# Kernel tuning notes

Hardware: AMD Instinct MI355X
Metric: run time of the kernel (lower is better)

Reference implementation:

```python
import jax, jax.numpy as jnp
import numpy as np

CODEBOOK_SIZE = 8192
CODEBOOK_DIM = 16
IN_DIM = 512


def setup_inputs() -> dict:
    key = jax.random.key(0)
    k1, k2, k3 = jax.random.split(key, 3)
    input_values = jax.random.normal(k1, (8, 4096, IN_DIM), dtype=jnp.float32)
    # xavier_uniform for Linear(IN_DIM -> CODEBOOK_DIM), weight shape (out, in) in torch
    limit = float(np.sqrt(6.0 / (IN_DIM + CODEBOOK_DIM)))
    proj_weight = jax.random.uniform(k2, (CODEBOOK_DIM, IN_DIM), dtype=jnp.float32, minval=-limit, maxval=limit)
    code_book = jax.random.normal(k3, (CODEBOOK_SIZE, CODEBOOK_DIM), dtype=jnp.float32)
    return {"input_values": input_values, "proj_weight": proj_weight, "code_book": code_book}


def reference(input_values, proj_weight, code_book):
    # targets: (B, L, d) = input @ W^T  (bias-free random projection)
    targets = jnp.einsum("bld,cd->blc", input_values, proj_weight)  # (B, L, 16)
    # Squared L2 distance via expansion ||t - c||^2 = ||t||^2 - 2 t.c + ||c||^2.
    # argmin is identical to argmin of the norm; avoids the (B,L,K,d) broadcast tensor.
    t_sq = jnp.sum(targets * targets, axis=-1, keepdims=True)        # (B, L, 1)
    c_sq = jnp.sum(code_book * code_book, axis=-1)                   # (K,)
    cross = jnp.einsum("blc,kc->blk", targets, code_book)            # (B, L, K)
    dist_sq = t_sq - 2.0 * cross + c_sq                              # (B, L, K)
    labels = jnp.argmin(dist_sq, axis=-1)                            # (B, L) int
    return labels
```

## Files before the change

kernel.cpp:

```cpp
#include <hip/hip_runtime.h>
#include <stdint.h>

#define IN_DIM 512
#define CB 8192
#define CD 16
#define NROWS 32768
#define DELTAQ 8e-3f
#define FMAXV 3.402823466e38f

typedef short bf16x8 __attribute__((ext_vector_type(8)));
typedef float f32x4 __attribute__((ext_vector_type(4)));

__device__ inline unsigned short f2bf(float x) {
    unsigned u = __float_as_uint(x);
    unsigned r = u + 0x7FFFu + ((u >> 16) & 1u);
    return (unsigned short)(r >> 16);
}
__device__ inline float bf2f(unsigned short h) { return __uint_as_float(((unsigned)h) << 16); }
__device__ inline unsigned umin32(unsigned a, unsigned b) { return a < b ? a : b; }
__device__ inline unsigned umax32(unsigned a, unsigned b) { return a > b ? a : b; }
__device__ inline unsigned long long shfl_xor_u64(unsigned long long x, int m) {
    double d = __shfl_xor(__longlong_as_double((long long)x), m, 64);
    return (unsigned long long)__double_as_longlong(d);
}
__device__ inline unsigned med3_u32(unsigned a, unsigned b, unsigned c) {
    unsigned d;
    asm("v_med3_u32 %0, %1, %2, %3" : "=v"(d) : "v"(a), "v"(b), "v"(c));
    return d;
}

__global__ __launch_bounds__(256) void prep_proj_kernel(const float* __restrict__ in,
                                                        const float* __restrict__ W,
                                                        float* __restrict__ partials,
                                                        const float* __restrict__ cb,
                                                        float* __restrict__ csq,
                                                        f32x4* __restrict__ csq4,
                                                        bf16x8* __restrict__ Bp,
                                                        int* __restrict__ counter) {
    __shared__ float4 LIN[2048];
    __shared__ float4 WL[16 * 33];
    int tid = threadIdx.x;

    if (blockIdx.x >= 2048) {
        int id = (blockIdx.x - 2048) * 256 + tid;
        if (id == 0) counter[0] = 0;
        if (id < CB) {
            const float4* p = (const float4*)(cb + (size_t)id * CD);
            float s = 0.f;
#pragma unroll
            for (int j = 0; j < 4; ++j) {
                float4 v = p[j];
                s += v.x * v.x + v.y * v.y + v.z * v.z + v.w * v.w;
            }
            csq[id] = s;
            float so = s + 256.0f;
            f32x4 v4 = {so, so, so, so};
            csq4[id] = v4;
        }
        int slot = id & 63;
        int nt = id >> 6;
        int q = slot >> 4;
        int n = nt * 16 + (slot & 15);
        int d0 = (q & 1) * 8;
        bool lo = (q < 2);
        const float* src = cb + (size_t)n * CD + d0;
        bf16x8 v;
#pragma unroll
        for (int j = 0; j < 8; ++j) {
            float x = src[j];
            unsigned short a = f2bf(x);
            unsigned short b = f2bf(x - bf2f(a));
            v[j] = (short)(lo ? a : b);
        }
        Bp[id] = v;
        return;
    }

    int lane = tid & 63;
    int dg = __builtin_amdgcn_readfirstlane(tid >> 6);
    int strip = blockIdx.x >> 2;
    int c = blockIdx.x & 3;
    int rowbase = strip * 64;
    const float4* inp4 = (const float4*)in;
    const float4* W4 = (const float4*)W;

#pragma unroll
    for (int u = 0; u < 2; ++u) {
        int f = tid + u * 256;
        int d = f >> 5, o = f & 31;
        WL[d * 33 + o] = W4[(size_t)d * 128 + c * 32 + o];
    }
#pragma unroll
    for (int u = 0; u < 8; ++u) {
        int f = tid + u * 256;
        int o = f & 31, r = f >> 5;
        LIN[o * 64 + (r ^ (o & 7))] = inp4[(size_t)(rowbase + r) * 128 + c * 32 + o];
    }
    __syncthreads();

    float acc[4];
#pragma unroll
    for (int i = 0; i < 4; ++i) acc[i] = 0.f;
#pragma unroll 4
    for (int j = 0; j < 32; ++j) {
        float4 v = LIN[j * 64 + (lane ^ (j & 7))];
#pragma unroll
        for (int i = 0; i < 4; ++i) {
            float4 w = WL[(4 * dg + i) * 33 + j];
            acc[i] += v.x * w.x + v.y * w.y + v.z * w.z + v.w * w.w;
        }
    }
    float* o = partials + (size_t)c * NROWS * CD + (size_t)(rowbase + lane) * CD + 4 * dg;
#pragma unroll
    for (int i = 0; i < 4; ++i) o[i] = acc[i];
}

__global__ __launch_bounds__(512, 4) void scan_kernel(
        const float* __restrict__ partials, const f32x4* __restrict__ csq4,
        const bf16x8* __restrict__ Bp, int* __restrict__ out,
        int* __restrict__ queue, int* __restrict__ counter) {
    __shared__ float tbuf[64][17];
    __shared__ unsigned long long m_k[64][8];
    __shared__ unsigned m_s2[64][8];

    int tid = threadIdx.x;
    int lane = tid & 63;
    int e = __builtin_amdgcn_readfirstlane(tid >> 6);
    int rowbase = blockIdx.x * 64;

#pragma unroll
    for (int u = 0; u < 2; ++u) {
        int f = tid + u * 512;
        int rr = f >> 4, d = f & 15;
        size_t idx = (size_t)(rowbase + rr) * CD + d;
        const size_t P = (size_t)NROWS * CD;
        float p0 = partials[idx];
        float p1 = partials[P + idx];
        float p2 = partials[2 * P + idx];
        float p3 = partials[3 * P + idx];
        tbuf[rr][d] = -2.f * (((p0 + p1) + p2) + p3);
    }
    __syncthreads();

    int q = lane >> 4;
    int col = lane & 15;
    int d0 = (q & 1) * 8;
    bool lo = (q < 2);

    bf16x8 A1[4], A2[4];
#pragma unroll
    for (int g = 0; g < 4; ++g) {
        int arow = 16 * g + col;
#pragma unroll
        for (int j = 0; j < 8; ++j) {
            float x = tbuf[arow][d0 + j];
            unsigned short t1 = f2bf(x);
            unsigned short t2 = f2bf(x - bf2f(t1));
            A1[g][j] = (short)t1;
            A2[g][j] = (short)(lo ? t2 : 0);
        }
    }

    unsigned s1[4][4], s2[4][4];
#pragma unroll
    for (int g = 0; g < 4; ++g)
#pragma unroll
        for (int r = 0; r < 4; ++r) { s1[g][r] = 0xFFFFFFFFu; s2[g][r] = 0xFFFFFFFFu; }

    int nt0 = e * 64;
    const bf16x8* pb = Bp + (size_t)nt0 * 64 + lane;
    const f32x4* csqp = csq4 + nt0 * 16 + col;

    for (int tc = 0; tc < 16; ++tc) {
        bf16x8 bv[4];
        f32x4 iv[4];
#pragma unroll
        for (int u = 0; u < 4; ++u) {
            bv[u] = pb[u * 64];
            iv[u] = csqp[u * 16];
        }
#pragma unroll
        for (int u = 0; u < 4; ++u) {
            unsigned tt = (unsigned)(tc * 4 + u);
#pragma unroll
            for (int g = 0; g < 4; ++g) {
                f32x4 acc = __builtin_amdgcn_mfma_f32_16x16x32_bf16(A1[g], bv[u], iv[u], 0, 0, 0);
                acc = __builtin_amdgcn_mfma_f32_16x16x32_bf16(A2[g], bv[u], acc, 0, 0, 0);
#pragma unroll
                for (int r = 0; r < 4; ++r) {
                    unsigned k = (__float_as_uint(acc[r]) & 0xFFFFFFC0u) | tt;
                    s2[g][r] = med3_u32(s1[g][r], s2[g][r], k);
                    s1[g][r] = umin32(s1[g][r], k);
                }
            }
        }
        pb += 256;
        csqp += 64;
    }

#pragma unroll
    for (int g = 0; g < 4; ++g)
#pragma unroll
        for (int r = 0; r < 4; ++r) {
            unsigned long long FK = ((unsigned long long)(s1[g][r] & 0xFFFFFFC0u) << 13)
                                  | ((unsigned long long)e << 10)
                                  | ((unsigned long long)(s1[g][r] & 63u) << 4)
                                  | (unsigned long long)col;
            unsigned s2q = s2[g][r] & 0xFFFFFFC0u;
#pragma unroll
            for (int m = 1; m < 16; m <<= 1) {
                unsigned long long oFK = shfl_xor_u64(FK, m);
                unsigned os2 = (unsigned)__shfl_xor((int)s2q, m, 64);
                unsigned qa = (unsigned)(FK >> 13);
                unsigned qb = (unsigned)(oFK >> 13);
                s2q = umin32(umin32(s2q, os2), umax32(qa, qb));
                FK = oFK < FK ? oFK : FK;
            }
            if (col == 0) {
                int rl = 16 * g + 4 * q + r;
                m_k[rl][e] = FK;
                m_s2[rl][e] = s2q;
            }
        }
    __syncthreads();

    if (tid < 64) {
        unsigned long long mFK = m_k[tid][0];
        unsigned g1 = (unsigned)(m_k[tid][0] >> 13);
        unsigned g2 = m_s2[tid][0];
#pragma unroll
        for (int ee = 1; ee < 8; ++ee) {
            unsigned long long F = m_k[tid][ee];
            unsigned u = (unsigned)(F >> 13);
            if (u < g1) { g2 = g1; g1 = u; } else { g2 = umin32(g2, u); }
            g2 = umin32(g2, m_s2[tid][ee]);
            mFK = F < mFK ? F : mFK;
        }
        int ccol = (int)(mFK & 15ull);
        int ctile = (int)((mFK >> 4) & 63ull);
        int ce = (int)((mFK >> 10) & 7ull);
        int row = rowbase + tid;
        out[row] = ((ce * 64 + ctile) << 4) | ccol;
        if (__uint_as_float(g2) - __uint_as_float(g1) < DELTAQ) {
            int pos = atomicAdd(counter, 1);
            queue[pos] = row;
        }
    }
}

__global__ __launch_bounds__(256) void fallback_kernel(const float* __restrict__ partials,
                                                       const float* __restrict__ cb,
                                                       const float* __restrict__ csq,
                                                       const int* __restrict__ queue,
                                                       const int* __restrict__ counter,
                                                       int* __restrict__ out) {
    __shared__ unsigned long long red[4];
    int nq = counter[0];
    int tid = threadIdx.x;
    int lane = tid & 63;
    int w = tid >> 6;

    for (int qi = blockIdx.x; qi < nq; qi += 2048) {
        int row = queue[qi];
        const size_t P = (size_t)NROWS * CD;
        size_t base = (size_t)row * CD;
        float tp[16];
#pragma unroll
        for (int d = 0; d < 16; ++d)
            tp[d] = -2.f * (((partials[base + d] + partials[P + base + d])
                             + partials[2 * P + base + d]) + partials[3 * P + base + d]);

        float best = FMAXV;
        int bidx = 0;
#pragma unroll 2
        for (int i = 0; i < 32; ++i) {
            int k = tid + 256 * i;
            const float* cp = cb + (size_t)k * CD;
            float s = csq[k];
#pragma unroll
            for (int d = 0; d < 16; ++d) s += tp[d] * cp[d];
            if (s < best) { best = s; bidx = k; }
        }
        unsigned u = __float_as_uint(best);
        u = (u & 0x80000000u) ? ~u : (u | 0x80000000u);
        unsigned long long key = ((unsigned long long)u << 32) | (unsigned)bidx;
#pragma unroll
        for (int m = 1; m < 64; m <<= 1) {
            unsigned long long o = shfl_xor_u64(key, m);
            key = o < key ? o : key;
        }
        if (lane == 0) red[w] = key;
        __syncthreads();
        if (tid == 0) {
            unsigned long long mm = red[0];
#pragma unroll
            for (int i = 1; i < 4; ++i) { unsigned long long x = red[i]; mm = x < mm ? x : mm; }
            out[row] = (int)(mm & 0xFFFFFFFFull);
        }
        __syncthreads();
    }
}

extern "C" void kernel_launch(void* const* d_in, const int* in_sizes, int n_in,
                              void* d_out, int out_size, void* d_ws, size_t ws_size,
                              hipStream_t stream) {
    const float* input = (const float*)d_in[0];
    const float* W     = (const float*)d_in[1];
    const float* cb    = (const float*)d_in[2];
    int* out = (int*)d_out;

    float*  partials = (float*)d_ws;
    float*  csq      = partials + 4 * (size_t)NROWS * CD;
    f32x4*  csq4     = (f32x4*)(csq + CB);
    bf16x8* Bp       = (bf16x8*)((float*)csq4 + 4 * CB);
    int*    counter  = (int*)(Bp + 32768);
    int*    queue    = counter + 16;

    prep_proj_kernel<<<2176, 256, 0, stream>>>(input, W, partials, cb, csq, csq4, Bp, counter);
    scan_kernel<<<NROWS / 64, 512, 0, stream>>>(partials, csq4, Bp, out, queue, counter);
    fallback_kernel<<<2048, 256, 0, stream>>>(partials, cb, csq, queue, counter, out);
}
```

Baseline: 162.8 us.

## Fuse input projection into scan kernel and drop partials buffer

Moves the 512->16 projection into the scan kernel, so each block computes its 64 rows' targets by looping over four input column chunks in shared memory before the codebook scan. This removes the separate projection pass and the 4-way partials buffer write and reread. Targets are also stored once, for the fallback kernel. In exchange, shared memory per block grows a lot, which may cut occupancy of the scan phase, and input loading is serialized inside fewer blocks.

After: 163.8 us. No clear change (+0.6%).

```diff
diff --git a/kernel.cpp b/kernel.cpp
--- a/kernel.cpp
+++ b/kernel.cpp
@@ -29,119 +29,103 @@
     return d;
 }
 
-__global__ __launch_bounds__(256) void prep_proj_kernel(const float* __restrict__ in,
-                                                        const float* __restrict__ W,
-                                                        float* __restrict__ partials,
-                                                        const float* __restrict__ cb,
-                                                        float* __restrict__ csq,
-                                                        f32x4* __restrict__ csq4,
-                                                        bf16x8* __restrict__ Bp,
-                                                        int* __restrict__ counter) {
-    __shared__ float4 LIN[2048];
-    __shared__ float4 WL[16 * 33];
-    int tid = threadIdx.x;
-
-    if (blockIdx.x >= 2048) {
-        int id = (blockIdx.x - 2048) * 256 + tid;
-        if (id == 0) counter[0] = 0;
-        if (id < CB) {
-            const float4* p = (const float4*)(cb + (size_t)id * CD);
-            float s = 0.f;
-#pragma unroll
-            for (int j = 0; j < 4; ++j) {
-                float4 v = p[j];
-                s += v.x * v.x + v.y * v.y + v.z * v.z + v.w * v.w;
-            }
-            csq[id] = s;
-            float so = s + 256.0f;
-            f32x4 v4 = {so, so, so, so};
-            csq4[id] = v4;
-        }
-        int slot = id & 63;
-        int nt = id >> 6;
-        int q = slot >> 4;
-        int n = nt * 16 + (slot & 15);
-        int d0 = (q & 1) * 8;
-        bool lo = (q < 2);
-        const float* src = cb + (size_t)n * CD + d0;
-        bf16x8 v;
-#pragma unroll
-        for (int j = 0; j < 8; ++j) {
-            float x = src[j];
-            unsigned short a = f2bf(x);
-            unsigned short b = f2bf(x - bf2f(a));
-            v[j] = (short)(lo ? a : b);
-        }
-        Bp[id] = v;
-        return;
-    }
-
-    int lane = tid & 63;
-    int dg = __builtin_amdgcn_readfirstlane(tid >> 6);
-    int strip = blockIdx.x >> 2;
-    int c = blockIdx.x & 3;
-    int rowbase = strip * 64;
-    const float4* inp4 = (const float4*)in;
-    const float4* W4 = (const float4*)W;
-
-#pragma unroll
-    for (int u = 0; u < 2; ++u) {
-        int f = tid + u * 256;
-        int d = f >> 5, o = f & 31;
-        WL[d * 33 + o] = W4[(size_t)d * 128 + c * 32 + o];
-    }
-#pragma unroll
-    for (int u = 0; u < 8; ++u) {
-        int f = tid + u * 256;
-        int o = f & 31, r = f >> 5;
-        LIN[o * 64 + (r ^ (o & 7))] = inp4[(size_t)(rowbase + r) * 128 + c * 32 + o];
-    }
-    __syncthreads();
-
-    float acc[4];
-#pragma unroll
-    for (int i = 0; i < 4; ++i) acc[i] = 0.f;
-#pragma unroll 4
-    for (int j = 0; j < 32; ++j) {
-        float4 v = LIN[j * 64 + (lane ^ (j & 7))];
-#pragma unroll
-        for (int i = 0; i < 4; ++i) {
-            float4 w = WL[(4 * dg + i) * 33 + j];
-            acc[i] += v.x * w.x + v.y * w.y + v.z * w.z + v.w * w.w;
-        }
-    }
-    float* o = partials + (size_t)c * NROWS * CD + (size_t)(rowbase + lane) * CD + 4 * dg;
-#pragma unroll
-    for (int i = 0; i < 4; ++i) o[i] = acc[i];
-}
-
-__global__ __launch_bounds__(512, 4) void scan_kernel(
-        const float* __restrict__ partials, const f32x4* __restrict__ csq4,
+__global__ __launch_bounds__(256) void prep_kernel(const float* __restrict__ cb,
+                                                   float* __restrict__ csq,
+                                                   f32x4* __restrict__ csq4,
+                                                   bf16x8* __restrict__ Bp,
+                                                   int* __restrict__ counter) {
+    int id = blockIdx.x * 256 + threadIdx.x;
+    if (id == 0) counter[0] = 0;
+    if (id < CB) {
+        const float4* p = (const float4*)(cb + (size_t)id * CD);
+        float s = 0.f;
+#pragma unroll
+        for (int j = 0; j < 4; ++j) {
+            float4 v = p[j];
+            s += v.x * v.x + v.y * v.y + v.z * v.z + v.w * v.w;
+        }
+        csq[id] = s;
+        float so = s + 256.0f;
+        f32x4 v4 = {so, so, so, so};
+        csq4[id] = v4;
+    }
+    int slot = id & 63;
+    int nt = id >> 6;
+    int q = slot >> 4;
+    int n = nt * 16 + (slot & 15);
+    int d0 = (q & 1) * 8;
+    bool lo = (q < 2);
+    const float* src = cb + (size_t)n * CD + d0;
+    bf16x8 v;
+#pragma unroll
+    for (int j = 0; j < 8; ++j) {
+        float x = src[j];
+        unsigned short a = f2bf(x);
+        unsigned short b = f2bf(x - bf2f(a));
+        v[j] = (short)(lo ? a : b);
+    }
+    Bp[id] = v;
+}
+
+__global__ __launch_bounds__(512, 4) void fused_kernel(
+        const float* __restrict__ in, const float* __restrict__ W,
+        float* __restrict__ tpout, const f32x4* __restrict__ csq4,
         const bf16x8* __restrict__ Bp, int* __restrict__ out,
         int* __restrict__ queue, int* __restrict__ counter) {
+    __shared__ float4 LIN[2048];
+    __shared__ float4 WL[16 * 129];
     __shared__ float tbuf[64][17];
     __shared__ unsigned long long m_k[64][8];
     __shared__ unsigned m_s2[64][8];
 
     int tid = threadIdx.x;
     int lane = tid & 63;
-    int e = __builtin_amdgcn_readfirstlane(tid >> 6);
+    int wv = __builtin_amdgcn_readfirstlane(tid >> 6);
     int rowbase = blockIdx.x * 64;
-
-#pragma unroll
-    for (int u = 0; u < 2; ++u) {
+    const float4* inp4 = (const float4*)in;
+    const float4* W4 = (const float4*)W;
+
+#pragma unroll
+    for (int u = 0; u < 4; ++u) {
         int f = tid + u * 512;
-        int rr = f >> 4, d = f & 15;
-        size_t idx = (size_t)(rowbase + rr) * CD + d;
-        const size_t P = (size_t)NROWS * CD;
-        float p0 = partials[idx];
-        float p1 = partials[P + idx];
-        float p2 = partials[2 * P + idx];
-        float p3 = partials[3 * P + idx];
-        tbuf[rr][d] = -2.f * (((p0 + p1) + p2) + p3);
+        int d = f >> 7, k = f & 127;
+        WL[d * 129 + k] = W4[(size_t)d * 128 + k];
+    }
+
+    float fold0 = 0.f, fold1 = 0.f;
+    for (int c = 0; c < 4; ++c) {
+        __syncthreads();
+#pragma unroll
+        for (int u = 0; u < 4; ++u) {
+            int f = tid + u * 512;
+            int o = f & 31, r = f >> 5;
+            LIN[o * 64 + (r ^ (o & 7))] = inp4[(size_t)(rowbase + r) * 128 + c * 32 + o];
+        }
+        __syncthreads();
+        float acc0 = 0.f, acc1 = 0.f;
+#pragma unroll 4
+        for (int j = 0; j < 32; ++j) {
+            float4 v = LIN[j * 64 + (lane ^ (j & 7))];
+            float4 w0 = WL[(2 * wv) * 129 + c * 32 + j];
+            float4 w1 = WL[(2 * wv + 1) * 129 + c * 32 + j];
+            acc0 += v.x * w0.x + v.y * w0.y + v.z * w0.z + v.w * w0.w;
+            acc1 += v.x * w1.x + v.y * w1.y + v.z * w1.z + v.w * w1.w;
+        }
+        fold0 += acc0;
+        fold1 += acc1;
+    }
+    float t0 = -2.f * fold0;
+    float t1 = -2.f * fold1;
+    tbuf[lane][2 * wv] = t0;
+    tbuf[lane][2 * wv + 1] = t1;
+    {
+        float* tp = tpout + (size_t)(rowbase + lane) * CD + 2 * wv;
+        tp[0] = t0;
+        tp[1] = t1;
     }
     __syncthreads();
 
+    int e = wv;
     int q = lane >> 4;
     int col = lane & 15;
     int d0 = (q & 1) * 8;
@@ -154,10 +138,10 @@
 #pragma unroll
         for (int j = 0; j < 8; ++j) {
             float x = tbuf[arow][d0 + j];
-            unsigned short t1 = f2bf(x);
-            unsigned short t2 = f2bf(x - bf2f(t1));
-            A1[g][j] = (short)t1;
-            A2[g][j] = (short)(lo ? t2 : 0);
+            unsigned short h1 = f2bf(x);
+            unsigned short h2 = f2bf(x - bf2f(h1));
+            A1[g][j] = (short)h1;
+            A2[g][j] = (short)(lo ? h2 : 0);
         }
     }
 
@@ -248,7 +232,7 @@
     }
 }
 
-__global__ __launch_bounds__(256) void fallback_kernel(const float* __restrict__ partials,
+__global__ __launch_bounds__(256) void fallback_kernel(const float* __restrict__ tpout,
                                                        const float* __restrict__ cb,
                                                        const float* __restrict__ csq,
                                                        const int* __restrict__ queue,
@@ -262,13 +246,10 @@
 
     for (int qi = blockIdx.x; qi < nq; qi += 2048) {
         int row = queue[qi];
-        const size_t P = (size_t)NROWS * CD;
-        size_t base = (size_t)row * CD;
+        const float* tpp = tpout + (size_t)row * CD;
         float tp[16];
 #pragma unroll
-        for (int d = 0; d < 16; ++d)
-            tp[d] = -2.f * (((partials[base + d] + partials[P + base + d])
-                             + partials[2 * P + base + d]) + partials[3 * P + base + d]);
+        for (int d = 0; d < 16; ++d) tp[d] = tpp[d];
 
         float best = FMAXV;
         int bidx = 0;
@@ -309,14 +290,14 @@
     const float* cb    = (const float*)d_in[2];
     int* out = (int*)d_out;
 
-    float*  partials = (float*)d_ws;
-    float*  csq      = partials + 4 * (size_t)NROWS * CD;
-    f32x4*  csq4     = (f32x4*)(csq + CB);
-    bf16x8* Bp       = (bf16x8*)((float*)csq4 + 4 * CB);
-    int*    counter  = (int*)(Bp + 32768);
-    int*    queue    = counter + 16;
-
-    prep_proj_kernel<<<2176, 256, 0, stream>>>(input, W, partials, cb, csq, csq4, Bp, counter);
-    scan_kernel<<<NROWS / 64, 512, 0, stream>>>(partials, csq4, Bp, out, queue, counter);
-    fallback_kernel<<<2048, 256, 0, stream>>>(partials, cb, csq, queue, counter, out);
-}
+    float*  tpout   = (float*)d_ws;
+    float*  csq     = tpout + (size_t)NROWS * CD;
+    f32x4*  csq4    = (f32x4*)(csq + CB);
+    bf16x8* Bp      = (bf16x8*)((float*)csq4 + 4 * CB);
+    int*    counter = (int*)(Bp + 32768);
+    int*    queue   = counter + 16;
+
+    prep_kernel<<<32768 / 256, 256, 0, stream>>>(cb, csq, csq4, Bp, counter);
+    fused_kernel<<<NROWS / 64, 512, 0, stream>>>(input, W, tpout, csq4, Bp, out, queue, counter);
+    fallback_kernel<<<2048, 256, 0, stream>>>(tpout, cb, csq, queue, counter, out);
+}
```
